# Kernel optimization log

Hardware: AMD Instinct MI355X
Metric: run time of the kernel (lower is better)

The kernel has to match this reference:

```python
import jax, jax.numpy as jnp
import numpy as np

N = 1048576        # number of time samples (rays)
V = 32             # num_videos
D = 32             # embedding_dim
F = 6              # num_frequencies
K = 2 * F + 1      # basis size: [1, sin(2^j*pi*t), cos(2^j*pi*t)]


def setup_inputs() -> dict:
    key = jax.random.key(0)
    k1, k2, k3 = jax.random.split(key, 3)
    times = jax.random.uniform(k1, (N, 1), dtype=jnp.float32)
    video_ids = jax.random.randint(k2, (N, 1), 0, V, dtype=jnp.int32)
    weights = jax.random.normal(k3, (V, D, K), dtype=jnp.float32)
    return {"times": times, "video_ids": video_ids, "weights": weights}


def _fourier_basis(t):
    # t: [N] -> [N, K] with basis [1, sin(2^j pi t), cos(2^j pi t)] j=0..F-1
    freqs = (2.0 ** jnp.arange(F, dtype=t.dtype)) * jnp.pi  # [F]
    ang = t[:, None] * freqs                                # [N, F]
    return jnp.concatenate(
        [jnp.ones_like(t)[:, None], jnp.sin(ang), jnp.cos(ang)], axis=-1
    )


def reference(times, video_ids, weights):
    shp = times.shape
    t = times.reshape(-1)                       # [N]
    vid = video_ids.reshape(-1).astype(jnp.int32)  # [N]
    basis = _fourier_basis(t)                   # [N, K]
    w = weights[vid]                            # gather: [N, D, K]
    emb = jnp.einsum('ndk,nk->nd', w, basis)    # [N, D]
    return emb.reshape((*shp[:-1], -1))
```

## Files before the change

### kernel.cpp

```cpp
#include <hip/hip_runtime.h>
#include <hip/hip_fp16.h>

#define NRAYS 1048576
#define NV 32
#define ND 32
#define NF 6
#define NK 13

typedef _Float16 h2 __attribute__((ext_vector_type(2)));
typedef float f4 __attribute__((ext_vector_type(4)));

__device__ __forceinline__ float fdot2acc(h2 a, h2 b, float c) {
#if __has_builtin(__builtin_amdgcn_fdot2)
    return __builtin_amdgcn_fdot2(a, b, c, false);
#else
    return c + (float)a.x * (float)b.x + (float)a.y * (float)b.y;
#endif
}

__device__ __forceinline__ h2 pack2(float a, float b) {
#if __has_builtin(__builtin_amdgcn_cvt_pkrtz)
    return __builtin_bit_cast(h2, __builtin_amdgcn_cvt_pkrtz(a, b));
#else
    h2 r; r.x = (_Float16)a; r.y = (_Float16)b; return r;
#endif
}

__device__ __forceinline__ float hwsin(float rev) {
#if __has_builtin(__builtin_amdgcn_sinf)
    return __builtin_amdgcn_sinf(rev);
#else
    return __sinf(6.28318530717958647692f * rev);
#endif
}
__device__ __forceinline__ float hwcos(float rev) {
#if __has_builtin(__builtin_amdgcn_cosf)
    return __builtin_amdgcn_cosf(rev);
#else
    return __cosf(6.28318530717958647692f * rev);
#endif
}

__global__ void pack_weights_kernel(const float* __restrict__ weights,
                                    unsigned* __restrict__ wpack)
{
    int j = blockIdx.x * 256 + threadIdx.x;
    if (j >= NV * 7 * 32) return;
    int v = j / 224;
    int r = j - v * 224;
    int i = r >> 5;
    int c = r & 31;
    int pos = c >> 2;
    int e = c & 3;
    int q = pos ^ (v & 7);
    int d = 4 * q + e;
    float w0 = weights[v * (ND * NK) + d * NK + 2 * i];
    float w1 = (2 * i + 1 < NK) ? weights[v * (ND * NK) + d * NK + 2 * i + 1] : 0.f;
    h2 p = pack2(w0, w1);
    wpack[j] = __builtin_bit_cast(unsigned, p);
}

__global__ __launch_bounds__(256, 5) void VideoEmbedding_kernel(
    const float* __restrict__ times,
    const int* __restrict__ vids,
    const unsigned* __restrict__ wpack,
    float* __restrict__ out)
{
    __shared__ _Float16 wl[NV * 7 * ND * 2];

    const int tid = threadIdx.x;

    {
        const uint4* src = reinterpret_cast<const uint4*>(wpack);
        uint4* dst = reinterpret_cast<uint4*>(wl);
#pragma unroll
        for (int j = 0; j < 7; ++j)
            dst[tid + j * 256] = src[tid + j * 256];
    }
    __syncthreads();

    const int q = tid & 7;
    const int gstride = (gridDim.x * 256) >> 3;
    int ray = ((blockIdx.x * 256) + tid) >> 3;

    float tt0 = times[ray];
    int vv0 = vids[ray];
    int r1 = min(ray + gstride, NRAYS - 1);
    float tt1 = times[r1];
    int vv1 = vids[r1];

    while (ray < NRAYS) {
        const int rayB = ray + gstride;
        const int rn0 = min(ray + 2 * gstride, NRAYS - 1);
        const int rn1 = min(ray + 3 * gstride, NRAYS - 1);
        const float tn0 = times[rn0], tn1 = times[rn1];
        const int vn0 = vids[rn0], vn1 = vids[rn1];

        const float tt[2] = {tt0, tt1};
        const int vv[2] = {vv0, vv1};
        f4 res[2];
#pragma unroll
        for (int u = 0; u < 2; ++u) {
            float sv[NF], cv[NF];
            sv[0] = hwsin(0.5f * tt[u]);
            cv[0] = hwcos(0.5f * tt[u]);
#pragma unroll
            for (int j = 1; j < NF; ++j) {
                float sj = sv[j - 1], cj = cv[j - 1];
                sv[j] = 2.f * sj * cj;
                cv[j] = fmaf(-2.f * sj, sj, 1.f);
            }

            h2 bp[7];
            bp[0] = pack2(1.0f, sv[0]);
            bp[1] = pack2(sv[1], sv[2]);
            bp[2] = pack2(sv[3], sv[4]);
            bp[3] = pack2(sv[5], cv[0]);
            bp[4] = pack2(cv[1], cv[2]);
            bp[5] = pack2(cv[3], cv[4]);
            bp[6] = pack2(cv[5], 0.0f);

            const unsigned pos = (unsigned)(q ^ (vv[u] & 7));
            const unsigned base = (unsigned)vv[u] * 448u + pos * 8u;
            float a0 = 0.f, a1 = 0.f, a2 = 0.f, a3 = 0.f;
#pragma unroll
            for (int i = 0; i < 7; ++i) {
                uint4 w = *reinterpret_cast<const uint4*>(&wl[base + i * 64]);
                a0 = fdot2acc(__builtin_bit_cast(h2, w.x), bp[i], a0);
                a1 = fdot2acc(__builtin_bit_cast(h2, w.y), bp[i], a1);
                a2 = fdot2acc(__builtin_bit_cast(h2, w.z), bp[i], a2);
                a3 = fdot2acc(__builtin_bit_cast(h2, w.w), bp[i], a3);
            }
            res[u].x = a0; res[u].y = a1; res[u].z = a2; res[u].w = a3;
        }

        __builtin_nontemporal_store(res[0],
            reinterpret_cast<f4*>(out) + (size_t)ray * 8 + q);
        if (rayB < NRAYS)
            __builtin_nontemporal_store(res[1],
                reinterpret_cast<f4*>(out) + (size_t)rayB * 8 + q);

        ray += 2 * gstride;
        tt0 = tn0; vv0 = vn0;
        tt1 = tn1; vv1 = vn1;
    }
}

extern "C" void kernel_launch(void* const* d_in, const int* in_sizes, int n_in,
                              void* d_out, int out_size, void* d_ws, size_t ws_size,
                              hipStream_t stream) {
    const float* times = (const float*)d_in[0];
    const int* vids = (const int*)d_in[1];
    const float* weights = (const float*)d_in[2];
    float* out = (float*)d_out;
    unsigned* wpack = (unsigned*)d_ws;

    hipLaunchKernelGGL(pack_weights_kernel, dim3(28), dim3(256), 0, stream,
                       weights, wpack);
    hipLaunchKernelGGL(VideoEmbedding_kernel, dim3(1280), dim3(256), 0, stream,
                       times, vids, wpack, out);
}
```

Measured before the change: 36.18 us.

## Stage per-block ray inputs in LDS and switch to fixed-size 512-thread blocks

Replaces the grid-stride loop (with register prefetch of times/vids) by fixed 1024-ray tiles per 512-thread block. Each block stages its tile's times and video ids into shared memory with coalesced loads, then loops 16 times over the tile. Output stores become regular stores instead of nontemporal ones. The aim is coalesced input loads and less per-iteration index overhead, but each block now reloads the 28KB weight table into LDS for only 1024 rays, and the software prefetch that overlapped loads with compute is gone.

```diff
diff --git a/kernel.cpp b/kernel.cpp
--- a/kernel.cpp
+++ b/kernel.cpp
@@ -41,6 +41,25 @@
 #endif
 }
 
+__device__ __forceinline__ void make_basis(float t, h2 bp[7]) {
+    float sv[NF], cv[NF];
+    sv[0] = hwsin(0.5f * t);
+    cv[0] = hwcos(0.5f * t);
+#pragma unroll
+    for (int j = 1; j < NF; ++j) {
+        float sj = sv[j - 1], cj = cv[j - 1];
+        sv[j] = 2.f * sj * cj;
+        cv[j] = fmaf(-2.f * sj, sj, 1.f);
+    }
+    bp[0] = pack2(1.0f, sv[0]);
+    bp[1] = pack2(sv[1], sv[2]);
+    bp[2] = pack2(sv[3], sv[4]);
+    bp[3] = pack2(sv[5], cv[0]);
+    bp[4] = pack2(cv[1], cv[2]);
+    bp[5] = pack2(cv[3], cv[4]);
+    bp[6] = pack2(cv[5], 0.0f);
+}
+
 __global__ void pack_weights_kernel(const float* __restrict__ weights,
                                     unsigned* __restrict__ wpack)
 {
@@ -56,93 +75,63 @@
     int d = 4 * q + e;
     float w0 = weights[v * (ND * NK) + d * NK + 2 * i];
     float w1 = (2 * i + 1 < NK) ? weights[v * (ND * NK) + d * NK + 2 * i + 1] : 0.f;
-    h2 p = pack2(w0, w1);
-    wpack[j] = __builtin_bit_cast(unsigned, p);
+    wpack[j] = __builtin_bit_cast(unsigned, pack2(w0, w1));
 }
 
-__global__ __launch_bounds__(256, 5) void VideoEmbedding_kernel(
+__global__ __launch_bounds__(512, 8) void VideoEmbedding_kernel(
     const float* __restrict__ times,
     const int* __restrict__ vids,
     const unsigned* __restrict__ wpack,
     float* __restrict__ out)
 {
     __shared__ _Float16 wl[NV * 7 * ND * 2];
+    __shared__ float s_t[1024];
+    __shared__ unsigned char s_v[1024];
 
     const int tid = threadIdx.x;
+    const int rbase = blockIdx.x * 1024;
 
     {
         const uint4* src = reinterpret_cast<const uint4*>(wpack);
         uint4* dst = reinterpret_cast<uint4*>(wl);
 #pragma unroll
-        for (int j = 0; j < 7; ++j)
-            dst[tid + j * 256] = src[tid + j * 256];
+        for (int j = 0; j < 4; ++j) {
+            int idx = tid + j * 512;
+            if (idx < 1792) dst[idx] = src[idx];
+        }
     }
+    s_t[tid] = times[rbase + tid];
+    s_t[tid + 512] = times[rbase + 512 + tid];
+    s_v[tid] = (unsigned char)vids[rbase + tid];
+    s_v[tid + 512] = (unsigned char)vids[rbase + 512 + tid];
     __syncthreads();
 
     const int q = tid & 7;
-    const int gstride = (gridDim.x * 256) >> 3;
-    int ray = ((blockIdx.x * 256) + tid) >> 3;
+    const int g = tid >> 3;
 
-    float tt0 = times[ray];
-    int vv0 = vids[ray];
-    int r1 = min(ray + gstride, NRAYS - 1);
-    float tt1 = times[r1];
-    int vv1 = vids[r1];
+    for (int p = 0; p < 16; ++p) {
+        const int slot = p * 64 + g;
+        const float t = s_t[slot];
+        const int v = s_v[slot];
 
-    while (ray < NRAYS) {
-        const int rayB = ray + gstride;
-        const int rn0 = min(ray + 2 * gstride, NRAYS - 1);
-        const int rn1 = min(ray + 3 * gstride, NRAYS - 1);
-        const float tn0 = times[rn0], tn1 = times[rn1];
-        const int vn0 = vids[rn0], vn1 = vids[rn1];
+        h2 bp[7];
+        make_basis(t, bp);
 
-        const float tt[2] = {tt0, tt1};
-        const int vv[2] = {vv0, vv1};
-        f4 res[2];
+        const unsigned base =
+            (unsigned)v * 448u + (unsigned)(q ^ (v & 7)) * 8u;
+        float a0 = 0.f, a1 = 0.f, a2 = 0.f, a3 = 0.f;
 #pragma unroll
-        for (int u = 0; u < 2; ++u) {
-            float sv[NF], cv[NF];
-            sv[0] = hwsin(0.5f * tt[u]);
-            cv[0] = hwcos(0.5f * tt[u]);
-#pragma unroll
-            for (int j = 1; j < NF; ++j) {
-                float sj = sv[j - 1], cj = cv[j - 1];
-                sv[j] = 2.f * sj * cj;
-                cv[j] = fmaf(-2.f * sj, sj, 1.f);
-            }
-
-            h2 bp[7];
-            bp[0] = pack2(1.0f, sv[0]);
-            bp[1] = pack2(sv[1], sv[2]);
-            bp[2] = pack2(sv[3], sv[4]);
-            bp[3] = pack2(sv[5], cv[0]);
-            bp[4] = pack2(cv[1], cv[2]);
-            bp[5] = pack2(cv[3], cv[4]);
-            bp[6] = pack2(cv[5], 0.0f);
-
-            const unsigned pos = (unsigned)(q ^ (vv[u] & 7));
-            const unsigned base = (unsigned)vv[u] * 448u + pos * 8u;
-            float a0 = 0.f, a1 = 0.f, a2 = 0.f, a3 = 0.f;
-#pragma unroll
-            for (int i = 0; i < 7; ++i) {
-                uint4 w = *reinterpret_cast<const uint4*>(&wl[base + i * 64]);
-                a0 = fdot2acc(__builtin_bit_cast(h2, w.x), bp[i], a0);
-                a1 = fdot2acc(__builtin_bit_cast(h2, w.y), bp[i], a1);
-                a2 = fdot2acc(__builtin_bit_cast(h2, w.z), bp[i], a2);
-                a3 = fdot2acc(__builtin_bit_cast(h2, w.w), bp[i], a3);
-            }
-            res[u].x = a0; res[u].y = a1; res[u].z = a2; res[u].w = a3;
+        for (int i = 0; i < 7; ++i) {
+            uint4 w = *reinterpret_cast<const uint4*>(&wl[base + i * 64]);
+            a0 = fdot2acc(__builtin_bit_cast(h2, w.x), bp[i], a0);
+            a1 = fdot2acc(__builtin_bit_cast(h2, w.y), bp[i], a1);
+            a2 = fdot2acc(__builtin_bit_cast(h2, w.z), bp[i], a2);
+            a3 = fdot2acc(__builtin_bit_cast(h2, w.w), bp[i], a3);
         }
 
-        __builtin_nontemporal_store(res[0],
-            reinterpret_cast<f4*>(out) + (size_t)ray * 8 + q);
-        if (rayB < NRAYS)
-            __builtin_nontemporal_store(res[1],
-                reinterpret_cast<f4*>(out) + (size_t)rayB * 8 + q);
-
-        ray += 2 * gstride;
-        tt0 = tn0; vv0 = vn0;
-        tt1 = tn1; vv1 = vn1;
+        f4 res;
+        res.x = a0; res.y = a1; res.z = a2; res.w = a3;
+        reinterpret_cast<f4*>(out)[(size_t)(rbase + slot) * 8 + q] = res;
     }
 }
 
@@ -157,6 +146,6 @@
 
     hipLaunchKernelGGL(pack_weights_kernel, dim3(28), dim3(256), 0, stream,
                        weights, wpack);
-    hipLaunchKernelGGL(VideoEmbedding_kernel, dim3(1280), dim3(256), 0, stream,
+    hipLaunchKernelGGL(VideoEmbedding_kernel, dim3(1024), dim3(512), 0, stream,
                        times, vids, wpack, out);
 }
```

Measured after the change: 33.97 us. -6.1%, faster.
